# Kernel optimization log

Hardware: AMD Instinct MI355X
Metric: run time of the kernel (lower is better)

The kernel has to match this reference:

```python
import jax, jax.numpy as jnp
import numpy as np

# Static config matching init_kwargs
WZ, WH, WW = 2, 6, 12          # window size
MZ, MH, MW = 4, 16, 15          # ceil(input_shape / window_size) for (8,96,180)
HEADS, DIM, B = 6, 192, 1
DH = DIM // HEADS
P = WZ * WH * WW                # 144 tokens per window
WN = MZ * MH * MW               # 960 windows
WT = MZ * MH                    # 64 window types
SCALE = DH ** -0.5
TABLE = WZ * WZ * WH * WH * (2 * WW - 1)  # 3312 bias entries


def _position_index():
    zi = np.arange(WZ); zj = -np.arange(WZ) * WZ
    hi = np.arange(WH); hj = -np.arange(WH) * WH
    w = np.arange(WW)
    c1 = np.stack(np.meshgrid(zi, hi, w, indexing='ij')).reshape(3, -1)  # (3, P)
    c2 = np.stack(np.meshgrid(zj, hj, w, indexing='ij')).reshape(3, -1)  # (3, P)
    coords = (c1[:, :, None] - c2[:, None, :]).transpose(1, 2, 0)        # (P, P, 3)
    coords[:, :, 2] += WW - 1
    coords[:, :, 1] *= 2 * WW - 1
    coords[:, :, 0] *= (2 * WW - 1) * WH * WH
    return coords.sum(-1).reshape(-1)  # (P*P,)

POS_IDX = jnp.asarray(_position_index())


def setup_inputs() -> dict:
    key = jax.random.key(0)
    ks = jax.random.split(key, 5)
    x = jax.random.normal(ks[0], (B * WN, P, DIM), dtype=jnp.float32)
    mask = jnp.zeros((WN, P, P), dtype=jnp.float32)
    w_qkv = jax.random.normal(ks[1], (DIM, 3 * DIM), dtype=jnp.float32) * 0.02
    w_proj = jax.random.normal(ks[2], (DIM, DIM), dtype=jnp.float32) * 0.02
    b_proj = jnp.zeros((DIM,), dtype=jnp.float32)
    bias_table = jax.random.normal(ks[3], (TABLE, WT, HEADS), dtype=jnp.float32) * 0.02
    return {"x": x, "mask": mask, "w_qkv": w_qkv, "w_proj": w_proj,
            "b_proj": b_proj, "bias_table": bias_table}


def reference(x, mask, w_qkv, w_proj, b_proj, bias_table):
    BN = x.shape[0]  # B*WN
    qkv = (x @ w_qkv).reshape(BN, P, 3, HEADS, DH).transpose(2, 0, 3, 1, 4)  # (3,BN,h,P,dh)
    q, k, v = SCALE * qkv[0], qkv[1], qkv[2]
    attn = jnp.einsum('bhid,bhjd->bhij', q, k)  # (BN, h, P, P)
    # (B mZ mH mW) h P P -> (B mW) (mZ mH) h P P
    attn = attn.reshape(B, MZ, MH, MW, HEADS, P, P)
    attn = attn.transpose(0, 3, 1, 2, 4, 5, 6).reshape(B * MW, WT, HEADS, P, P)
    # gather earth-specific bias: (P*P, WT, h) -> (WT, h, P, P)
    bias = bias_table[POS_IDX].reshape(P, P, WT, HEADS).transpose(2, 3, 0, 1)
    attn = attn + bias  # broadcast over (B mW)
    # back to (B mZ mH mW) h P P
    attn = attn.reshape(B, MW, MZ, MH, HEADS, P, P)
    attn = attn.transpose(0, 2, 3, 1, 4, 5, 6).reshape(B, WN, HEADS, P, P)
    attn = attn + mask[None, :, None]  # (1, wN, 1, P, P)
    attn = jax.nn.softmax(attn, axis=-1).reshape(B * WN, HEADS, P, P)
    out = jnp.einsum('bhij,bhjd->bhid', attn, v)           # (BN, h, P, dh)
    out = out.transpose(0, 2, 1, 3).reshape(BN, P, DIM)    # merge heads
    return out @ w_proj + b_proj
```

## Files before the change

### kernel.cpp

```cpp
#include <hip/hip_runtime.h>

#define HEADS 6
#define DIM 192
#define DH 32
#define PW 144
#define WN 960
#define MWD 15
#define NTOK (WN*PW)
#define SCALE 0.17677669529663687f
#define LOG2E 1.4426950408889634f
#define SCALE2 (SCALE * LOG2E)

typedef __attribute__((ext_vector_type(8))) short bf16x8;
typedef __attribute__((ext_vector_type(4))) short bf16x4;
typedef __attribute__((ext_vector_type(4))) float f32x4;

#define MFMA16(a,b,c) __builtin_amdgcn_mfma_f32_16x16x32_bf16(a,b,c,0,0,0)

__device__ __forceinline__ unsigned short f2bf(float f) {
    unsigned int u = __builtin_bit_cast(unsigned int, f);
    u += 0x7fffu + ((u >> 16) & 1u);
    return (unsigned short)(u >> 16);
}
__device__ __forceinline__ float bf2f(unsigned short s) {
    unsigned int u = ((unsigned int)s) << 16;
    return __builtin_bit_cast(float, u);
}

__global__ void prep_weights(const float* __restrict__ wqkv,
                             const float* __restrict__ wproj,
                             unsigned short* __restrict__ wqkvT,
                             unsigned short* __restrict__ wprojT) {
    int t = blockIdx.x * 256 + threadIdx.x;
    if (t < 576 * 192) {
        int n = t / 192, k = t % 192;
        wqkvT[t] = f2bf(wqkv[k * 576 + n]);
    } else {
        int t2 = t - 576 * 192;
        int n = t2 / 192, k = t2 % 192;
        wprojT[t2] = f2bf(wproj[k * 192 + n]);
    }
}

__global__ void prep_bias(const float* __restrict__ table,
                          unsigned short* __restrict__ bias_d) {
    int t = blockIdx.x * 256 + threadIdx.x;
    int j = t % 144;
    int i = (t / 144) % 144;
    int h = (t / 20736) % 6;
    int wt = t / 124416;
    int z1 = i / 72, h1 = (i / 12) % 6, w1 = i % 12;
    int z2 = j / 72, h2 = (j / 12) % 6, w2 = j % 12;
    int pos = (z1 + 2 * z2) * 828 + (h1 + 6 * h2) * 23 + (w1 - w2 + 11);
    bias_d[t] = f2bf(table[pos * 384 + wt * 6 + h] * LOG2E);
}

__global__ __launch_bounds__(256) void qkv_gemm(
        const float* __restrict__ x, const unsigned short* __restrict__ wqkvT,
        unsigned short* __restrict__ qb, unsigned short* __restrict__ kb,
        unsigned short* __restrict__ vtb) {
    __shared__ unsigned short A[64 * 200];
    __shared__ unsigned short Bt[96 * 200];
    int bid = blockIdx.x;
    int r8 = bid & 7, s = bid >> 3;
    int nblk = s % 6;
    int mtile = r8 * 270 + s / 6;
    int tid = threadIdx.x;

    const float* xp = x + (long long)mtile * (64 * 192);
    #pragma unroll
    for (int it = 0; it < 6; ++it) {
        int c = tid + it * 256;
        int row = c / 24, c8 = (c % 24) * 8;
        const float* p = xp + c * 8;
        f32x4 v0 = *(const f32x4*)p;
        f32x4 v1 = *(const f32x4*)(p + 4);
        bf16x8 o;
        o[0] = (short)f2bf(v0[0]); o[1] = (short)f2bf(v0[1]);
        o[2] = (short)f2bf(v0[2]); o[3] = (short)f2bf(v0[3]);
        o[4] = (short)f2bf(v1[0]); o[5] = (short)f2bf(v1[1]);
        o[6] = (short)f2bf(v1[2]); o[7] = (short)f2bf(v1[3]);
        *(bf16x8*)&A[row * 200 + c8] = o;
    }
    const unsigned short* wp = wqkvT + nblk * (96 * 192);
    #pragma unroll
    for (int it = 0; it < 9; ++it) {
        int c = tid + it * 256;
        int row = c / 24, c8 = (c % 24) * 8;
        *(bf16x8*)&Bt[row * 200 + c8] = *(const bf16x8*)(wp + c * 8);
    }
    __syncthreads();

    int lane = tid & 63, wv = tid >> 6;
    int l16 = lane & 15, quad = lane >> 4;
    f32x4 acc[6];
    #pragma unroll
    for (int i = 0; i < 6; ++i) acc[i] = (f32x4){0.f, 0.f, 0.f, 0.f};

    #pragma unroll
    for (int kc = 0; kc < 6; ++kc) {
        bf16x8 af = *(const bf16x8*)&A[(wv * 16 + l16) * 200 + kc * 32 + quad * 8];
        #pragma unroll
        for (int ct = 0; ct < 6; ++ct) {
            bf16x8 bfr = *(const bf16x8*)&Bt[(ct * 16 + l16) * 200 + kc * 32 + quad * 8];
            acc[ct] = MFMA16(af, bfr, acc[ct]);
        }
    }

    int token0 = mtile * 64 + wv * 16 + quad * 4;
    int win = token0 / 144;
    int p0 = token0 - win * 144;
    #pragma unroll
    for (int ct = 0; ct < 6; ++ct) {
        int c0 = nblk * 96 + ct * 16;
        int which = c0 / 192;
        int head = (c0 % 192) / 32;
        int d = (c0 % 32) + l16;
        if (which == 0) {
            int base = ((win * 6 + head) * 144 + p0) * 32 + d;
            #pragma unroll
            for (int r = 0; r < 4; ++r) qb[base + r * 32] = f2bf(acc[ct][r]);
        } else if (which == 1) {
            int base = ((win * 6 + head) * 144 + p0) * 32 + d;
            #pragma unroll
            for (int r = 0; r < 4; ++r) kb[base + r * 32] = f2bf(acc[ct][r]);
        } else {
            int base = ((win * 6 + head) * 32 + d) * 144 + p0;
            bf16x4 o;
            #pragma unroll
            for (int r = 0; r < 4; ++r) o[r] = (short)f2bf(acc[ct][r]);
            *(bf16x4*)&vtb[base] = o;
        }
    }
}

__global__ __launch_bounds__(192, 3) void attn(
        const unsigned short* __restrict__ qb, const unsigned short* __restrict__ kb,
        const unsigned short* __restrict__ vtb, const unsigned short* __restrict__ bias_d,
        const float* __restrict__ mask, unsigned short* __restrict__ Ob) {
    __shared__ unsigned short Kl[144 * 40];
    __shared__ unsigned short Vt[32 * 168];
    __shared__ unsigned short Pl[3 * 16 * 168];

    int bx = blockIdx.x;
    int r8 = bx & 7, s = bx >> 3;
    int h = s % 6;
    int win = r8 * 120 + s / 6;
    int wt = win / MWD;
    int tid = threadIdx.x;
    int lane = tid & 63, wv = tid >> 6;
    int l16 = lane & 15, quad = lane >> 4;

    int qoff = (win * 6 + h) * (144 * 32);
    #pragma unroll
    for (int it = 0; it < 3; ++it) {
        int c = tid + it * 192;
        int row = c >> 2, c8 = (c & 3) * 8;
        *(bf16x8*)&Kl[row * 40 + c8] = *(const bf16x8*)(kb + qoff + c * 8);
        int vr = c / 18, vc = (c % 18) * 8;
        *(bf16x8*)&Vt[vr * 168 + vc] = *(const bf16x8*)(vtb + qoff + c * 8);
    }
    bf16x8 qreg[3];
    #pragma unroll
    for (int rt = 0; rt < 3; ++rt)
        qreg[rt] = *(const bf16x8*)(qb + qoff + (((wv * 3 + rt) * 16) + l16) * 32 + quad * 8);
    {
        int row = lane >> 2, ch = lane & 3;
        *(bf16x4*)&Pl[wv * 2688 + row * 168 + 144 + ch * 4] = (bf16x4){0, 0, 0, 0};
    }
    if (tid < 96) {
        int row = tid / 3, off = 144 + (tid % 3) * 8;
        *(bf16x8*)&Vt[row * 168 + off] = (bf16x8){0, 0, 0, 0, 0, 0, 0, 0};
    }
    __syncthreads();

    const float* maskp = mask + win * 20736;
    const unsigned short* biasp = bias_d + (wt * 6 + h) * 20736;
    const f32x4 z = {0.f, 0.f, 0.f, 0.f};
    int pb = wv * 2688;

    #pragma unroll
    for (int rt = 0; rt < 3; ++rt) {
        int i0 = (wv * 3 + rt) * 16;
        int ibase = (i0 + quad * 4) * 144 + l16;
        f32x4 bm[9];
        #pragma unroll
        for (int ct = 0; ct < 9; ++ct) {
            #pragma unroll
            for (int r = 0; r < 4; ++r) {
                int off = ibase + r * 144 + ct * 16;
                bm[ct][r] = fmaf(maskp[off], LOG2E, bf2f(biasp[off]));
            }
        }
        bf16x8 aq = qreg[rt];
        f32x4 sreg[9];
        #pragma unroll
        for (int ct = 0; ct < 9; ++ct) {
            bf16x8 bk = *(const bf16x8*)&Kl[(ct * 16 + l16) * 40 + quad * 8];
            sreg[ct] = MFMA16(aq, bk, z);
        }
        #pragma unroll
        for (int ct = 0; ct < 9; ++ct) {
            #pragma unroll
            for (int r = 0; r < 4; ++r)
                sreg[ct][r] = fmaf(sreg[ct][r], SCALE2, bm[ct][r]);
        }
        float inv[4];
        #pragma unroll
        for (int r = 0; r < 4; ++r) {
            float mx = sreg[0][r];
            #pragma unroll
            for (int ct = 1; ct < 9; ++ct) mx = fmaxf(mx, sreg[ct][r]);
            #pragma unroll
            for (int off = 1; off < 16; off <<= 1) mx = fmaxf(mx, __shfl_xor(mx, off, 64));
            float sum = 0.f;
            #pragma unroll
            for (int ct = 0; ct < 9; ++ct) {
                float e = __builtin_amdgcn_exp2f(sreg[ct][r] - mx);
                sreg[ct][r] = e; sum += e;
            }
            #pragma unroll
            for (int off = 1; off < 16; off <<= 1) sum += __shfl_xor(sum, off, 64);
            inv[r] = __builtin_amdgcn_rcpf(sum);
        }
        #pragma unroll
        for (int ct = 0; ct < 9; ++ct) {
            #pragma unroll
            for (int r = 0; r < 4; ++r)
                Pl[pb + (quad * 4 + r) * 168 + ct * 16 + l16] = f2bf(sreg[ct][r]);
        }
        f32x4 o0 = z, o1 = z;
        #pragma unroll
        for (int kc = 0; kc < 5; ++kc) {
            bf16x8 ap = *(const bf16x8*)&Pl[pb + l16 * 168 + kc * 32 + quad * 8];
            bf16x8 b0 = *(const bf16x8*)&Vt[l16 * 168 + kc * 32 + quad * 8];
            bf16x8 b1 = *(const bf16x8*)&Vt[(16 + l16) * 168 + kc * 32 + quad * 8];
            o0 = MFMA16(ap, b0, o0);
            o1 = MFMA16(ap, b1, o1);
        }
        #pragma unroll
        for (int r = 0; r < 4; ++r) {
            int i = i0 + quad * 4 + r;
            int ob = (win * 144 + i) * 192 + h * 32 + l16;
            Ob[ob] = f2bf(o0[r] * inv[r]);
            Ob[ob + 16] = f2bf(o1[r] * inv[r]);
        }
    }
}

__global__ __launch_bounds__(256) void out_gemm(
        const unsigned short* __restrict__ Ob, const unsigned short* __restrict__ wprojT,
        const float* __restrict__ bproj, float* __restrict__ out) {
    __shared__ unsigned short A[64 * 200];
    __shared__ unsigned short Bt[96 * 200];
    int bid = blockIdx.x;
    int r8 = bid & 7, s = bid >> 3;
    int nblk = s % 2;
    int mtile = r8 * 270 + s / 2;
    int tid = threadIdx.x;

    const unsigned short* op = Ob + (long long)mtile * (64 * 192);
    #pragma unroll
    for (int it = 0; it < 6; ++it) {
        int c = tid + it * 256;
        int row = c / 24, c8 = (c % 24) * 8;
        *(bf16x8*)&A[row * 200 + c8] = *(const bf16x8*)(op + c * 8);
    }
    const unsigned short* wp = wprojT + nblk * (96 * 192);
    #pragma unroll
    for (int it = 0; it < 9; ++it) {
        int c = tid + it * 256;
        int row = c / 24, c8 = (c % 24) * 8;
        *(bf16x8*)&Bt[row * 200 + c8] = *(const bf16x8*)(wp + c * 8);
    }
    __syncthreads();

    int lane = tid & 63, wv = tid >> 6;
    int l16 = lane & 15, quad = lane >> 4;
    f32x4 acc[6];
    #pragma unroll
    for (int i = 0; i < 6; ++i) acc[i] = (f32x4){0.f, 0.f, 0.f, 0.f};
    #pragma unroll
    for (int kc = 0; kc < 6; ++kc) {
        bf16x8 af = *(const bf16x8*)&A[(wv * 16 + l16) * 200 + kc * 32 + quad * 8];
        #pragma unroll
        for (int ct = 0; ct < 6; ++ct) {
            bf16x8 bfr = *(const bf16x8*)&Bt[(ct * 16 + l16) * 200 + kc * 32 + quad * 8];
            acc[ct] = MFMA16(af, bfr, acc[ct]);
        }
    }
    int token0 = mtile * 64 + wv * 16 + quad * 4;
    #pragma unroll
    for (int ct = 0; ct < 6; ++ct) {
        int c = nblk * 96 + ct * 16 + l16;
        float bp = bproj[c];
        #pragma unroll
        for (int r = 0; r < 4; ++r)
            out[(token0 + r) * 192 + c] = acc[ct][r] + bp;
    }
}

extern "C" void kernel_launch(void* const* d_in, const int* in_sizes, int n_in,
                              void* d_out, int out_size, void* d_ws, size_t ws_size,
                              hipStream_t stream) {
    const float* x     = (const float*)d_in[0];
    const float* mask  = (const float*)d_in[1];
    const float* wqkv  = (const float*)d_in[2];
    const float* wproj = (const float*)d_in[3];
    const float* bproj = (const float*)d_in[4];
    const float* btab  = (const float*)d_in[5];
    float* out = (float*)d_out;

    char* ws = (char*)d_ws;
    unsigned short* Ob     = (unsigned short*)(ws + 0);
    unsigned short* qb     = (unsigned short*)(ws + 53084160);
    unsigned short* kb     = (unsigned short*)(ws + 106168320);
    unsigned short* vtb    = (unsigned short*)(ws + 159252480);
    unsigned short* bias_d = (unsigned short*)(ws + 212336640);
    unsigned short* wqkvT  = (unsigned short*)(ws + 228261888);
    unsigned short* wprojT = (unsigned short*)(ws + 228483072);

    prep_weights<<<576, 256, 0, stream>>>(wqkv, wproj, wqkvT, wprojT);
    prep_bias<<<31104, 256, 0, stream>>>(btab, bias_d);
    qkv_gemm<<<12960, 256, 0, stream>>>(x, wqkvT, qb, kb, vtb);
    attn<<<5760, 192, 0, stream>>>(qb, kb, vtb, bias_d, mask, Ob);
    out_gemm<<<4320, 256, 0, stream>>>(Ob, wprojT, bproj, out);
}
```

Before: 519.7 us.

## Skip zero mask reads per window, pre-cast x, drop LDS staging in GEMMs

Adds a prepass that flags windows whose mask is all zero, so the attention kernel reads only the bias for those windows and skips the fp32 mask load. The mask check runs on device for every call, so nonzero masks still take the full path. Also adds a separate kernel that casts x to bf16 once, so qkv_gemm no longer recasts it for each of its six column blocks. Both GEMMs now load MFMA fragments straight from global memory instead of staging them in LDS. The flags are kept in the output buffer and the bf16 x copy shares workspace with Ob, which relies on out_gemm overwriting the flags and on kernel ordering.

```diff
diff --git a/kernel.cpp b/kernel.cpp
--- a/kernel.cpp
+++ b/kernel.cpp
@@ -55,54 +55,62 @@
     bias_d[t] = f2bf(table[pos * 384 + wt * 6 + h] * LOG2E);
 }
 
+__global__ __launch_bounds__(256) void prep_cast(const float* __restrict__ x,
+                                                 unsigned short* __restrict__ xb) {
+    long long c = (long long)blockIdx.x * 256 + threadIdx.x;
+    const float* p = x + c * 8;
+    f32x4 v0 = *(const f32x4*)p;
+    f32x4 v1 = *(const f32x4*)(p + 4);
+    bf16x8 o;
+    o[0] = (short)f2bf(v0[0]); o[1] = (short)f2bf(v0[1]);
+    o[2] = (short)f2bf(v0[2]); o[3] = (short)f2bf(v0[3]);
+    o[4] = (short)f2bf(v1[0]); o[5] = (short)f2bf(v1[1]);
+    o[6] = (short)f2bf(v1[2]); o[7] = (short)f2bf(v1[3]);
+    *(bf16x8*)(xb + c * 8) = o;
+}
+
+__global__ __launch_bounds__(256) void prep_maskflag(const float* __restrict__ mask,
+                                                     int* __restrict__ flags) {
+    __shared__ int any;
+    if (threadIdx.x == 0) any = 0;
+    __syncthreads();
+    const float* mp = mask + blockIdx.x * 20736;
+    int nz = 0;
+    for (int c = threadIdx.x; c < 5184; c += 256) {
+        f32x4 v = *(const f32x4*)(mp + c * 4);
+        if (v[0] != 0.f || v[1] != 0.f || v[2] != 0.f || v[3] != 0.f) nz = 1;
+    }
+    if (nz) atomicOr(&any, 1);
+    __syncthreads();
+    if (threadIdx.x == 0) flags[blockIdx.x] = any;
+}
+
 __global__ __launch_bounds__(256) void qkv_gemm(
-        const float* __restrict__ x, const unsigned short* __restrict__ wqkvT,
+        const unsigned short* __restrict__ xb, const unsigned short* __restrict__ wqkvT,
         unsigned short* __restrict__ qb, unsigned short* __restrict__ kb,
         unsigned short* __restrict__ vtb) {
-    __shared__ unsigned short A[64 * 200];
-    __shared__ unsigned short Bt[96 * 200];
     int bid = blockIdx.x;
     int r8 = bid & 7, s = bid >> 3;
     int nblk = s % 6;
     int mtile = r8 * 270 + s / 6;
     int tid = threadIdx.x;
-
-    const float* xp = x + (long long)mtile * (64 * 192);
-    #pragma unroll
-    for (int it = 0; it < 6; ++it) {
-        int c = tid + it * 256;
-        int row = c / 24, c8 = (c % 24) * 8;
-        const float* p = xp + c * 8;
-        f32x4 v0 = *(const f32x4*)p;
-        f32x4 v1 = *(const f32x4*)(p + 4);
-        bf16x8 o;
-        o[0] = (short)f2bf(v0[0]); o[1] = (short)f2bf(v0[1]);
-        o[2] = (short)f2bf(v0[2]); o[3] = (short)f2bf(v0[3]);
-        o[4] = (short)f2bf(v1[0]); o[5] = (short)f2bf(v1[1]);
-        o[6] = (short)f2bf(v1[2]); o[7] = (short)f2bf(v1[3]);
-        *(bf16x8*)&A[row * 200 + c8] = o;
-    }
-    const unsigned short* wp = wqkvT + nblk * (96 * 192);
-    #pragma unroll
-    for (int it = 0; it < 9; ++it) {
-        int c = tid + it * 256;
-        int row = c / 24, c8 = (c % 24) * 8;
-        *(bf16x8*)&Bt[row * 200 + c8] = *(const bf16x8*)(wp + c * 8);
-    }
-    __syncthreads();
-
     int lane = tid & 63, wv = tid >> 6;
     int l16 = lane & 15, quad = lane >> 4;
+
+    const unsigned short* Ap = xb + (long long)mtile * (64 * 192)
+                               + (wv * 16 + l16) * 192 + quad * 8;
+    const unsigned short* Bp = wqkvT + (nblk * 96 + l16) * 192 + quad * 8;
+
     f32x4 acc[6];
     #pragma unroll
     for (int i = 0; i < 6; ++i) acc[i] = (f32x4){0.f, 0.f, 0.f, 0.f};
 
     #pragma unroll
     for (int kc = 0; kc < 6; ++kc) {
-        bf16x8 af = *(const bf16x8*)&A[(wv * 16 + l16) * 200 + kc * 32 + quad * 8];
+        bf16x8 af = *(const bf16x8*)(Ap + kc * 32);
         #pragma unroll
         for (int ct = 0; ct < 6; ++ct) {
-            bf16x8 bfr = *(const bf16x8*)&Bt[(ct * 16 + l16) * 200 + kc * 32 + quad * 8];
+            bf16x8 bfr = *(const bf16x8*)(Bp + ct * (16 * 192) + kc * 32);
             acc[ct] = MFMA16(af, bfr, acc[ct]);
         }
     }
@@ -137,7 +145,8 @@
 __global__ __launch_bounds__(192, 3) void attn(
         const unsigned short* __restrict__ qb, const unsigned short* __restrict__ kb,
         const unsigned short* __restrict__ vtb, const unsigned short* __restrict__ bias_d,
-        const float* __restrict__ mask, unsigned short* __restrict__ Ob) {
+        const float* __restrict__ mask, const int* __restrict__ mflags,
+        unsigned short* __restrict__ Ob) {
     __shared__ unsigned short Kl[144 * 40];
     __shared__ unsigned short Vt[32 * 168];
     __shared__ unsigned short Pl[3 * 16 * 168];
@@ -172,6 +181,7 @@
         int row = tid / 3, off = 144 + (tid % 3) * 8;
         *(bf16x8*)&Vt[row * 168 + off] = (bf16x8){0, 0, 0, 0, 0, 0, 0, 0};
     }
+    int mflag = mflags[win];
     __syncthreads();
 
     const float* maskp = mask + win * 20736;
@@ -184,12 +194,23 @@
         int i0 = (wv * 3 + rt) * 16;
         int ibase = (i0 + quad * 4) * 144 + l16;
         f32x4 bm[9];
-        #pragma unroll
-        for (int ct = 0; ct < 9; ++ct) {
-            #pragma unroll
-            for (int r = 0; r < 4; ++r) {
-                int off = ibase + r * 144 + ct * 16;
-                bm[ct][r] = fmaf(maskp[off], LOG2E, bf2f(biasp[off]));
+        if (mflag) {
+            #pragma unroll
+            for (int ct = 0; ct < 9; ++ct) {
+                #pragma unroll
+                for (int r = 0; r < 4; ++r) {
+                    int off = ibase + r * 144 + ct * 16;
+                    bm[ct][r] = fmaf(maskp[off], LOG2E, bf2f(biasp[off]));
+                }
+            }
+        } else {
+            #pragma unroll
+            for (int ct = 0; ct < 9; ++ct) {
+                #pragma unroll
+                for (int r = 0; r < 4; ++r) {
+                    int off = ibase + r * 144 + ct * 16;
+                    bm[ct][r] = bf2f(biasp[off]);
+                }
             }
         }
         bf16x8 aq = qreg[rt];
@@ -251,44 +272,32 @@
 __global__ __launch_bounds__(256) void out_gemm(
         const unsigned short* __restrict__ Ob, const unsigned short* __restrict__ wprojT,
         const float* __restrict__ bproj, float* __restrict__ out) {
-    __shared__ unsigned short A[64 * 200];
-    __shared__ unsigned short Bt[96 * 200];
     int bid = blockIdx.x;
     int r8 = bid & 7, s = bid >> 3;
     int nblk = s % 2;
     int mtile = r8 * 270 + s / 2;
     int tid = threadIdx.x;
-
-    const unsigned short* op = Ob + (long long)mtile * (64 * 192);
-    #pragma unroll
-    for (int it = 0; it < 6; ++it) {
-        int c = tid + it * 256;
-        int row = c / 24, c8 = (c % 24) * 8;
-        *(bf16x8*)&A[row * 200 + c8] = *(const bf16x8*)(op + c * 8);
-    }
-    const unsigned short* wp = wprojT + nblk * (96 * 192);
-    #pragma unroll
-    for (int it = 0; it < 9; ++it) {
-        int c = tid + it * 256;
-        int row = c / 24, c8 = (c % 24) * 8;
-        *(bf16x8*)&Bt[row * 200 + c8] = *(const bf16x8*)(wp + c * 8);
-    }
-    __syncthreads();
-
     int lane = tid & 63, wv = tid >> 6;
     int l16 = lane & 15, quad = lane >> 4;
+
+    const unsigned short* Ap = Ob + (long long)mtile * (64 * 192)
+                               + (wv * 16 + l16) * 192 + quad * 8;
+    const unsigned short* Bp = wprojT + (nblk * 96 + l16) * 192 + quad * 8;
+
     f32x4 acc[6];
     #pragma unroll
     for (int i = 0; i < 6; ++i) acc[i] = (f32x4){0.f, 0.f, 0.f, 0.f};
+
     #pragma unroll
     for (int kc = 0; kc < 6; ++kc) {
-        bf16x8 af = *(const bf16x8*)&A[(wv * 16 + l16) * 200 + kc * 32 + quad * 8];
+        bf16x8 af = *(const bf16x8*)(Ap + kc * 32);
         #pragma unroll
         for (int ct = 0; ct < 6; ++ct) {
-            bf16x8 bfr = *(const bf16x8*)&Bt[(ct * 16 + l16) * 200 + kc * 32 + quad * 8];
+            bf16x8 bfr = *(const bf16x8*)(Bp + ct * (16 * 192) + kc * 32);
             acc[ct] = MFMA16(af, bfr, acc[ct]);
         }
     }
+
     int token0 = mtile * 64 + wv * 16 + quad * 4;
     #pragma unroll
     for (int ct = 0; ct < 6; ++ct) {
@@ -310,8 +319,10 @@
     const float* bproj = (const float*)d_in[4];
     const float* btab  = (const float*)d_in[5];
     float* out = (float*)d_out;
+    int* mflags = (int*)d_out;
 
     char* ws = (char*)d_ws;
+    unsigned short* xb     = (unsigned short*)(ws + 0);
     unsigned short* Ob     = (unsigned short*)(ws + 0);
     unsigned short* qb     = (unsigned short*)(ws + 53084160);
     unsigned short* kb     = (unsigned short*)(ws + 106168320);
@@ -322,7 +333,9 @@
 
     prep_weights<<<576, 256, 0, stream>>>(wqkv, wproj, wqkvT, wprojT);
     prep_bias<<<31104, 256, 0, stream>>>(btab, bias_d);
-    qkv_gemm<<<12960, 256, 0, stream>>>(x, wqkvT, qb, kb, vtb);
-    attn<<<5760, 192, 0, stream>>>(qb, kb, vtb, bias_d, mask, Ob);
+    prep_maskflag<<<960, 256, 0, stream>>>(mask, mflags);
+    prep_cast<<<12960, 256, 0, stream>>>(x, xb);
+    qkv_gemm<<<12960, 256, 0, stream>>>(xb, wqkvT, qb, kb, vtb);
+    attn<<<5760, 192, 0, stream>>>(qb, kb, vtb, bias_d, mask, mflags, Ob);
     out_gemm<<<4320, 256, 0, stream>>>(Ob, wprojT, bproj, out);
 }
```

Measured after the change: 663.1 us. 27.6% more time.
